# Kernel tuning notes

Hardware: AMD Instinct MI355X
Metric: run time of the kernel (lower is better)

## Reference

```python
import jax, jax.numpy as jnp
import numpy as np

B, C, H, W = 8, 96, 56, 56
N = H * W
K = 9
COUT = 2 * C  # 192


def setup_inputs() -> dict:
    key = jax.random.key(0)
    ks = jax.random.split(key, 12)
    s = 0.05
    inp = {
        "x": jax.random.normal(ks[0], (B, C, H, W), jnp.float32),
        "kmap_w": jax.random.normal(ks[1], (C, 500), jnp.float32) * s,
        "kmap_b": jnp.zeros((500,), jnp.float32),
        "kfc_w": jax.random.normal(ks[2], (500, 64), jnp.float32) * s,
        "kfc_b": jnp.zeros((64,), jnp.float32),
        "kmu_w": jax.random.normal(ks[3], (64, 32), jnp.float32) * s,
        "kmu_b": jnp.zeros((32,), jnp.float32),
        "kdec_w": jax.random.normal(ks[4], (32, K), jnp.float32) * s,
        "kdec_b": jnp.zeros((K,), jnp.float32),
        "ec1_w": jax.random.normal(ks[5], (2 * C, C), jnp.float32) * s,
        "ec1_b": jnp.zeros((C,), jnp.float32),
        "ec2_w": jax.random.normal(ks[6], (2 * C, C), jnp.float32) * s,
        "ec2_b": jnp.zeros((C,), jnp.float32),
        "fc_w": jax.random.normal(ks[7], (C, COUT), jnp.float32) * s,
        "fc_b": jnp.zeros((COUT,), jnp.float32),
        "io_w": jax.random.normal(ks[8], (C, COUT), jnp.float32) * s,
        "io_b": jnp.zeros((COUT,), jnp.float32),
        "up_w": jax.random.normal(ks[9], (2 * COUT, COUT), jnp.float32) * s,
        "up_b": jnp.zeros((COUT,), jnp.float32),
    }
    return inp


def reference(x, kmap_w, kmap_b, kfc_w, kfc_b, kmu_w, kmu_b, kdec_w, kdec_b,
              ec1_w, ec1_b, ec2_w, ec2_b, fc_w, fc_b, io_w, io_b, up_w, up_b):
    b, c, h, w = x.shape
    n = h * w
    xf = x.reshape(b, c, n).transpose(0, 2, 1)  # [B, N, C]

    # ---- dense kNN graph (dilation=1, deterministic) ----
    sq = jnp.sum(xf * xf, axis=-1)  # [B, N]
    dist = sq[:, :, None] - 2.0 * jnp.einsum('bnc,bmc->bnm', xf, xf) + sq[:, None, :]
    _, nn_idx = jax.lax.top_k(-dist, K)  # [B, N, K] local neighbor indices

    nodes = xf.reshape(b * n, c)  # flat node features

    # ---- VAE-like K predictor -> per-node kept-degree (non-differentiable) ----
    hK = nodes @ kmap_w + kmap_b
    hK = jax.nn.relu(hK @ kfc_w + kfc_b)
    mu = hK @ kmu_w + kmu_b
    logits = mu @ kdec_w + kdec_b  # [B*N, K]
    k_int = jnp.argmax(logits, axis=1)  # in [0, K-1]

    # edge mask: keep first k_int[i] of node i's K edges
    edge_mask = (jnp.arange(K)[None, :] < k_int[:, None]).reshape(-1)  # [B*N*K]
    emask = edge_mask.astype(nodes.dtype)[:, None]

    # flatten edges with per-batch node offsets (local -> global indices)
    offs = (jnp.arange(b) * n)[:, None, None]
    src = (nn_idx + offs).reshape(-1)              # x_j
    dst = jnp.repeat(jnp.arange(b * n), K)         # x_i (center)

    def edge_conv(feat, wgt, bias):
        xi = feat[dst]
        xj = feat[src]
        msg = jnp.concatenate([xi, xj - xi], axis=-1) @ wgt + bias
        msg = msg * emask  # pruned edges contribute 0 to 'add' aggregation
        return jax.ops.segment_sum(msg, dst, num_segments=b * n)

    h1 = jax.nn.relu(edge_conv(nodes, ec1_w, ec1_b))
    h2 = edge_conv(h1, ec2_w, ec2_b)
    agg = h2 @ fc_w + fc_b                 # EdgeAgg output [B*N, COUT]

    xio = nodes @ io_w + io_b              # inOutFC
    upd = jax.nn.relu(jnp.concatenate([xio, agg], axis=-1) @ up_w + up_b)

    out = upd.reshape(b, n, 2 * c).transpose(0, 2, 1).reshape(b, 2 * c, h, w)
    return out
```

## Files before the change

kernel.cpp:

```cpp
#include <hip/hip_runtime.h>

#define NODES 25088
#define NB 8
#define NPB 3136
#define C 96
#define KNN 9
#define COUT 192
#define MSPLIT 4
#define T12 12
#define NCAND (MSPLIT * T12)

typedef float f32x4 __attribute__((ext_vector_type(4)));
typedef float f32x16 __attribute__((ext_vector_type(16)));
typedef short s16x8 __attribute__((ext_vector_type(8)));

__device__ __forceinline__ unsigned short f2bf(float x) {
  unsigned u = __float_as_uint(x);
  return (unsigned short)((u + 0x7fffu + ((u >> 16) & 1u)) >> 16);
}
__device__ __forceinline__ float bf2f(unsigned short h) {
  return __uint_as_float(((unsigned)h) << 16);
}

__global__ __launch_bounds__(256) void txsq_kernel(
    const float* __restrict__ x, float* __restrict__ xf, float* __restrict__ sq,
    unsigned short* __restrict__ xh, unsigned short* __restrict__ xl) {
  __shared__ float t[96][33];
  int tid = threadIdx.x;
  int b = blockIdx.y;
  int n0 = blockIdx.x * 32;
  const float* xb = x + (size_t)b * C * NPB;
  int tn = tid & 31, tc = tid >> 5;
#pragma unroll
  for (int i = 0; i < 12; i++) {
    int c = tc + i * 8;
    t[c][tn] = xb[(size_t)c * NPB + n0 + tn];
  }
  __syncthreads();
#pragma unroll
  for (int k = 0; k < 3; k++) {
    int it = tid + k * 256;
    int nl = it / 24, c4 = it % 24;
    int node = b * NPB + n0 + nl;
    float4 v;
    v.x = t[4 * c4 + 0][nl];
    v.y = t[4 * c4 + 1][nl];
    v.z = t[4 * c4 + 2][nl];
    v.w = t[4 * c4 + 3][nl];
    ushort4 h, l;
    h.x = f2bf(v.x); l.x = f2bf(v.x - bf2f(h.x));
    h.y = f2bf(v.y); l.y = f2bf(v.y - bf2f(h.y));
    h.z = f2bf(v.z); l.z = f2bf(v.z - bf2f(h.z));
    h.w = f2bf(v.w); l.w = f2bf(v.w - bf2f(h.w));
    ((float4*)(xf + (size_t)node * C))[c4] = v;
    ((ushort4*)(xh + (size_t)node * C))[c4] = h;
    ((ushort4*)(xl + (size_t)node * C))[c4] = l;
  }
  if (tid < 32) {
    int node = b * NPB + n0 + tid;
    float s = 0.f;
#pragma unroll
    for (int i = 0; i < 24; i++) {
      float4 v;
      v.x = t[4 * i + 0][tid];
      v.y = t[4 * i + 1][tid];
      v.z = t[4 * i + 2][tid];
      v.w = t[4 * i + 3][tid];
      s += v.x * v.x + v.y * v.y + v.z * v.z + v.w * v.w;
    }
    sq[node] = s;
  }
}

__global__ void fold_all_kernel(
    const float* __restrict__ kmap_w, const float* __restrict__ kmap_b,
    const float* __restrict__ kfc_w, const float* __restrict__ kfc_b,
    const float* __restrict__ kmu_w, const float* __restrict__ kmu_b,
    const float* __restrict__ kdec_w, const float* __restrict__ kdec_b,
    const float* __restrict__ ec1_w, const float* __restrict__ ec2_w,
    const float* __restrict__ io_w, const float* __restrict__ io_b,
    const float* __restrict__ fc_w, const float* __restrict__ fc_b,
    const float* __restrict__ up_w, const float* __restrict__ up_b,
    float* __restrict__ WkP, float* __restrict__ bkP, float* __restrict__ WdP,
    float* __restrict__ bdP, float* __restrict__ bPf,
    unsigned short* __restrict__ B1h, unsigned short* __restrict__ B1l,
    unsigned short* __restrict__ B2h, unsigned short* __restrict__ B2l,
    unsigned short* __restrict__ BFh, unsigned short* __restrict__ BFl) {
  __shared__ float sh[4][64];
  int bid = blockIdx.x, tid = threadIdx.x;
  int tx = tid & 63, ty = tid >> 6;
  if (bid < 96) {
    int m = bid;
    float acc = 0.f;
    for (int k = ty; k < 500; k += 4) acc += kmap_w[m * 500 + k] * kfc_w[k * 64 + tx];
    sh[ty][tx] = acc;
    __syncthreads();
    if (ty == 0) WkP[m * 64 + tx] = sh[0][tx] + sh[1][tx] + sh[2][tx] + sh[3][tx];
  } else if (bid == 96) {
    float acc = 0.f;
    for (int k = ty; k < 500; k += 4) acc += kmap_b[k] * kfc_w[k * 64 + tx];
    sh[ty][tx] = acc;
    __syncthreads();
    if (ty == 0) bkP[tx] = sh[0][tx] + sh[1][tx] + sh[2][tx] + sh[3][tx] + kfc_b[tx];
  } else if (bid < 161) {
    int m = bid - 97;
    float acc = 0.f;
    if (tx < 9) {
      for (int k = ty; k < 32; k += 4) acc += kmu_w[m * 32 + k] * kdec_w[k * 9 + tx];
    }
    sh[ty][tx] = acc;
    __syncthreads();
    if (ty == 0 && tx < 9) WdP[m * 9 + tx] = sh[0][tx] + sh[1][tx] + sh[2][tx] + sh[3][tx];
  } else if (bid == 161) {
    float acc = 0.f;
    if (tx < 9) {
      for (int k = ty; k < 32; k += 4) acc += kmu_b[k] * kdec_w[k * 9 + tx];
    }
    sh[ty][tx] = acc;
    __syncthreads();
    if (ty == 0 && tx < 9) bdP[tx] = sh[0][tx] + sh[1][tx] + sh[2][tx] + sh[3][tx] + kdec_b[tx];
  } else if (bid < 234) {
    int t = (bid - 162) * 256 + tid;
    int n = t / 192, k = t % 192;
    float v = ec1_w[(size_t)k * 96 + n];
    if (k < 96) v -= ec1_w[(size_t)(k + 96) * 96 + n];
    unsigned short h = f2bf(v);
    B1h[t] = h;
    B1l[t] = f2bf(v - bf2f(h));
  } else if (bid < 306) {
    int t = (bid - 234) * 256 + tid;
    int n = t / 192, k = t % 192;
    float v = ec2_w[(size_t)k * 96 + n];
    if (k < 96) v -= ec2_w[(size_t)(k + 96) * 96 + n];
    unsigned short h = f2bf(v);
    B2h[t] = h;
    B2l[t] = f2bf(v - bf2f(h));
  } else if (bid < 594) {
    int r = bid - 306;
    int m = r / 3, n = (r % 3) * 64 + tx;
    float acc = 0.f;
    for (int k = ty; k < 192; k += 4) acc += io_w[m * 192 + k] * up_w[(size_t)k * 192 + n];
    sh[ty][tx] = acc;
    __syncthreads();
    if (ty == 0) {
      float v = sh[0][tx] + sh[1][tx] + sh[2][tx] + sh[3][tx];
      unsigned short h = f2bf(v);
      BFh[(size_t)n * 192 + m] = h;
      BFl[(size_t)n * 192 + m] = f2bf(v - bf2f(h));
    }
  } else if (bid < 882) {
    int r = bid - 594;
    int m = r / 3, n = (r % 3) * 64 + tx;
    float acc = 0.f;
    for (int k = ty; k < 192; k += 4)
      acc += fc_w[m * 192 + k] * up_w[(size_t)(192 + k) * 192 + n];
    sh[ty][tx] = acc;
    __syncthreads();
    if (ty == 0) {
      float v = sh[0][tx] + sh[1][tx] + sh[2][tx] + sh[3][tx];
      unsigned short h = f2bf(v);
      BFh[(size_t)n * 192 + 96 + m] = h;
      BFl[(size_t)n * 192 + 96 + m] = f2bf(v - bf2f(h));
    }
  } else {
    if (tid < 192) {
      float acc = up_b[tid];
      for (int k = 0; k < 192; k++) {
        acc += io_b[k] * up_w[k * 192 + tid];
        acc += fc_b[k] * up_w[(192 + k) * 192 + tid];
      }
      bPf[tid] = acc;
    }
  }
}

__global__ __launch_bounds__(256) void gemmhead_kernel(
    const float* __restrict__ A0, const float* __restrict__ B,
    const float* __restrict__ bias, const float* __restrict__ WdP,
    const float* __restrict__ bdP, int* __restrict__ kint,
    float* __restrict__ rs) {
  __shared__ float As[16][68];
  __shared__ float Bs[16][68];
  __shared__ float hs[64][68];
  __shared__ float wd[576];
  __shared__ float bd[9];
  int tid = threadIdx.x;
  int tx = tid & 15, ty = tid >> 4;
  int row0 = blockIdx.x * 64;
  for (int f = tid; f < 576; f += 256) wd[f] = WdP[f];
  if (tid < 9) bd[tid] = bdP[tid];
  float acc[4][4] = {};
  int ai = tid >> 2;
  int ak = (tid & 3) * 4;
  int bk = tid >> 4;
  int bj = (tid & 15) * 4;

  for (int k0 = 0; k0 < 96; k0 += 16) {
    {
      int r = row0 + ai;
      float4 v = *(const float4*)(A0 + (size_t)r * 96 + k0 + ak);
      As[ak + 0][ai] = v.x;
      As[ak + 1][ai] = v.y;
      As[ak + 2][ai] = v.z;
      As[ak + 3][ai] = v.w;
    }
    {
      int kg = k0 + bk;
      float4 v = *(const float4*)(B + (size_t)kg * 64 + bj);
      *(float4*)&Bs[bk][bj] = v;
    }
    __syncthreads();
#pragma unroll
    for (int kk = 0; kk < 16; kk++) {
      float4 av = *(const float4*)&As[kk][ty * 4];
      float4 bv = *(const float4*)&Bs[kk][tx * 4];
      acc[0][0] += av.x * bv.x; acc[0][1] += av.x * bv.y; acc[0][2] += av.x * bv.z; acc[0][3] += av.x * bv.w;
      acc[1][0] += av.y * bv.x; acc[1][1] += av.y * bv.y; acc[1][2] += av.y * bv.z; acc[1][3] += av.y * bv.w;
      acc[2][0] += av.z * bv.x; acc[2][1] += av.z * bv.y; acc[2][2] += av.z * bv.z; acc[2][3] += av.z * bv.w;
      acc[3][0] += av.w * bv.x; acc[3][1] += av.w * bv.y; acc[3][2] += av.w * bv.z; acc[3][3] += av.w * bv.w;
    }
    __syncthreads();
  }
#pragma unroll
  for (int ii = 0; ii < 4; ii++) {
#pragma unroll
    for (int jj = 0; jj < 4; jj++) {
      int j = tx * 4 + jj;
      hs[ty * 4 + ii][j] = fmaxf(acc[ii][jj] + bias[j], 0.f);
    }
  }
  __syncthreads();
  if (tid < 64) {
    int node = row0 + tid;
    const float4* hp = (const float4*)hs[tid];
    float4 h[16];
#pragma unroll
    for (int i = 0; i < 16; i++) h[i] = hp[i];
    float best = -3.4e38f;
    int bi = 0;
#pragma unroll
    for (int n = 0; n < 9; n++) {
      float a = bd[n];
#pragma unroll
      for (int k = 0; k < 16; k++) {
        float4 hv = h[k];
        a += hv.x * wd[(4 * k + 0) * 9 + n] + hv.y * wd[(4 * k + 1) * 9 + n] +
             hv.z * wd[(4 * k + 2) * 9 + n] + hv.w * wd[(4 * k + 3) * 9 + n];
      }
      if (a > best) { best = a; bi = n; }
    }
    kint[node] = bi;
    rs[node] = (float)bi;
  }
}

__device__ __forceinline__ void ce(float& a, float& b) {
  float lo = fminf(a, b);
  b = fmaxf(a, b);
  a = lo;
}

__device__ __forceinline__ void sort16(float* s) {
  ce(s[0], s[1]); ce(s[2], s[3]); ce(s[0], s[2]); ce(s[1], s[3]); ce(s[1], s[2]);
  ce(s[4], s[5]); ce(s[6], s[7]); ce(s[4], s[6]); ce(s[5], s[7]); ce(s[5], s[6]);
  ce(s[0], s[4]); ce(s[1], s[5]); ce(s[2], s[6]); ce(s[3], s[7]);
  ce(s[2], s[4]); ce(s[3], s[5]);
  ce(s[1], s[2]); ce(s[3], s[4]); ce(s[5], s[6]);
  ce(s[8], s[9]); ce(s[10], s[11]); ce(s[8], s[10]); ce(s[9], s[11]); ce(s[9], s[10]);
  ce(s[12], s[13]); ce(s[14], s[15]); ce(s[12], s[14]); ce(s[13], s[15]); ce(s[13], s[14]);
  ce(s[8], s[12]); ce(s[9], s[13]); ce(s[10], s[14]); ce(s[11], s[15]);
  ce(s[10], s[12]); ce(s[11], s[13]);
  ce(s[9], s[10]); ce(s[11], s[12]); ce(s[13], s[14]);
  ce(s[0], s[8]); ce(s[1], s[9]); ce(s[2], s[10]); ce(s[3], s[11]);
  ce(s[4], s[12]); ce(s[5], s[13]); ce(s[6], s[14]); ce(s[7], s[15]);
  ce(s[4], s[8]); ce(s[5], s[9]); ce(s[6], s[10]); ce(s[7], s[11]);
  ce(s[2], s[4]); ce(s[3], s[5]); ce(s[6], s[8]); ce(s[7], s[9]);
  ce(s[10], s[12]); ce(s[11], s[13]);
  ce(s[1], s[2]); ce(s[3], s[4]); ce(s[5], s[6]); ce(s[7], s[8]);
  ce(s[9], s[10]); ce(s[11], s[12]); ce(s[13], s[14]);
}

__device__ __forceinline__ void bmerge12(float* fd, const float* s) {
  float L[12];
#pragma unroll
  for (int i = 0; i < 12; i++) L[i] = fminf(fd[i], s[11 - i]);
  ce(L[0], L[8]); ce(L[1], L[9]); ce(L[2], L[10]); ce(L[3], L[11]);
  ce(L[4], L[8]); ce(L[5], L[9]); ce(L[6], L[10]); ce(L[7], L[11]);
  ce(L[0], L[2]); ce(L[1], L[3]); ce(L[4], L[6]); ce(L[5], L[7]);
  ce(L[8], L[10]); ce(L[9], L[11]);
  ce(L[0], L[1]); ce(L[2], L[3]); ce(L[4], L[5]); ce(L[6], L[7]);
  ce(L[8], L[9]); ce(L[10], L[11]);
#pragma unroll
  for (int i = 0; i < 12; i++) fd[i] = L[i];
}

__global__ __launch_bounds__(256) void knn_mfma_kernel(
    const unsigned short* __restrict__ xh, const unsigned short* __restrict__ xl,
    const float* __restrict__ sq, int* __restrict__ pk_i) {
  __shared__ __align__(16) float smem_f[6784];
  unsigned short* mhA = (unsigned short*)smem_f;
  unsigned short* mhB = (unsigned short*)(smem_f + 3328);
  float* sqsA = smem_f + 6656;
  float* sqsB = smem_f + 6720;
  int tid = threadIdx.x;
  int lane = tid & 63, wv = tid >> 6;
  int wm = wv >> 1, wq = wv & 1;
  int b = blockIdx.y, z = blockIdx.z;
  int q0 = blockIdx.x * 64;
  int bbase = b * NPB;
  int t0 = (z * 49) / MSPLIT, t1 = ((z + 1) * 49) / MSPLIT;

  int koff = (lane >> 5) * 8;
  int qrow = bbase + q0 + wq * 32 + (lane & 31);
  s16x8 bqh[6], bql[6];
  {
    const unsigned short* ph = xh + (size_t)qrow * 96 + koff;
    const unsigned short* pl = xl + (size_t)qrow * 96 + koff;
#pragma unroll
    for (int kc = 0; kc < 6; kc++) {
      bqh[kc] = *(const s16x8*)(ph + kc * 16);
      bql[kc] = *(const s16x8*)(pl + kc * 16);
    }
  }
  float sqr = sq[qrow];

  float fd[12];
#pragma unroll
  for (int k = 0; k < 12; k++) fd[k] = 3.4e38f;

  int srow = tid >> 1;
  int tloc = srow >> 6;
  int rrow = srow & 63;
  int sseg = (tid & 1) * 48;
  int soff = rrow * 104 + sseg;
  unsigned short* mhd = tloc ? mhB : mhA;

  s16x8 st[6];
  float stq = 0.f;
  {
    int tA = t0 + tloc;
    int ts = (tA < t1) ? tA : (t1 - 1);
    const unsigned short* gh = xh + (size_t)(bbase + ts * 64 + rrow) * 96 + sseg;
#pragma unroll
    for (int i = 0; i < 6; i++) st[i] = *(const s16x8*)(gh + i * 8);
    if (tid < 128) {
      int tq = t0 + (tid >> 6);
      int tqs = (tq < t1) ? tq : (t1 - 1);
      stq = sq[bbase + tqs * 64 + (tid & 63)];
    }
  }

  int sqbase = wm * 32 + 4 * (lane >> 5);
  int mrow = wm * 32 + (lane & 31);
  int np = (t1 - t0 + 1) >> 1;

  for (int p = 0; p < np; p++) {
    int ta = t0 + 2 * p, tb = ta + 1;
    __syncthreads();
#pragma unroll
    for (int i = 0; i < 6; i++) *(s16x8*)(mhd + soff + i * 8) = st[i];
    if (tid < 128) ((tid >> 6) ? sqsB : sqsA)[tid & 63] = stq;
    __syncthreads();

    {
      int tn = t0 + 2 * (p + 1) + tloc;
      int ts = (tn < t1) ? tn : (t1 - 1);
      const unsigned short* gh = xh + (size_t)(bbase + ts * 64 + rrow) * 96 + sseg;
#pragma unroll
      for (int i = 0; i < 6; i++) st[i] = *(const s16x8*)(gh + i * 8);
      if (tid < 128) {
        int tq = t0 + 2 * (p + 1) + (tid >> 6);
        int tqs = (tq < t1) ? tq : (t1 - 1);
        stq = sq[bbase + tqs * 64 + (tid & 63)];
      }
    }

    {
      f32x16 acc = (f32x16){0.f, 0.f, 0.f, 0.f, 0.f, 0.f, 0.f, 0.f,
                            0.f, 0.f, 0.f, 0.f, 0.f, 0.f, 0.f, 0.f};
#pragma unroll
      for (int kc = 0; kc < 6; kc++) {
        s16x8 amh = *(const s16x8*)(mhA + mrow * 104 + kc * 16 + koff);
        acc = __builtin_amdgcn_mfma_f32_32x32x16_bf16(amh, bqh[kc], acc, 0, 0, 0);
        acc = __builtin_amdgcn_mfma_f32_32x32x16_bf16(amh, bql[kc], acc, 0, 0, 0);
      }
      f32x4 sm0 = *(const f32x4*)(sqsA + sqbase);
      f32x4 sm1 = *(const f32x4*)(sqsA + sqbase + 8);
      f32x4 sm2 = *(const f32x4*)(sqsA + sqbase + 16);
      f32x4 sm3 = *(const f32x4*)(sqsA + sqbase + 24);
      int lbase = (ta - t0) * 64;
      float cs[16];
#pragma unroll
      for (int reg = 0; reg < 16; reg++) {
        int g = reg >> 2, e = reg & 3;
        float sqm = (g == 0) ? sm0[e] : (g == 1) ? sm1[e] : (g == 2) ? sm2[e] : sm3[e];
        int mloc = wm * 32 + e + 8 * g + 4 * (lane >> 5);
        float d = fmaf(-2.f, acc[reg], sqr + sqm);
        unsigned u = (__float_as_uint(d) & 0xFFFFFC00u) | (unsigned)(lbase + mloc);
        cs[reg] = __uint_as_float(u);
      }
      sort16(cs);
      bmerge12(fd, cs);
    }
    if (tb < t1) {
      f32x16 acc = (f32x16){0.f, 0.f, 0.f, 0.f, 0.f, 0.f, 0.f, 0.f,
                            0.f, 0.f, 0.f, 0.f, 0.f, 0.f, 0.f, 0.f};
#pragma unroll
      for (int kc = 0; kc < 6; kc++) {
        s16x8 amh = *(const s16x8*)(mhB + mrow * 104 + kc * 16 + koff);
        acc = __builtin_amdgcn_mfma_f32_32x32x16_bf16(amh, bqh[kc], acc, 0, 0, 0);
        acc = __builtin_amdgcn_mfma_f32_32x32x16_bf16(amh, bql[kc], acc, 0, 0, 0);
      }
      f32x4 sm0 = *(const f32x4*)(sqsB + sqbase);
      f32x4 sm1 = *(const f32x4*)(sqsB + sqbase + 8);
      f32x4 sm2 = *(const f32x4*)(sqsB + sqbase + 16);
      f32x4 sm3 = *(const f32x4*)(sqsB + sqbase + 24);
      int lbase = (tb - t0) * 64;
      float cs[16];
#pragma unroll
      for (int reg = 0; reg < 16; reg++) {
        int g = reg >> 2, e = reg & 3;
        float sqm = (g == 0) ? sm0[e] : (g == 1) ? sm1[e] : (g == 2) ? sm2[e] : sm3[e];
        int mloc = wm * 32 + e + 8 * g + 4 * (lane >> 5);
        float d = fmaf(-2.f, acc[reg], sqr + sqm);
        unsigned u = (__float_as_uint(d) & 0xFFFFFC00u) | (unsigned)(lbase + mloc);
        cs[reg] = __uint_as_float(u);
      }
      sort16(cs);
      bmerge12(fd, cs);
    }
  }

  __syncthreads();
  float* cd = smem_f;
#pragma unroll
  for (int k = 0; k < 12; k++) cd[(wv * 64 + lane) * 13 + k] = fd[k];
  __syncthreads();
  if (wv == 0) {
    int wva = lane >> 5, ql = lane & 31;
    int ra = wva * 64 + ql, rb = wva * 64 + ql + 32;
    int rc = (wva + 2) * 64 + ql, rd = (wva + 2) * 64 + ql + 32;
    float A[12], B[12];
#pragma unroll
    for (int k = 0; k < 12; k++) { A[k] = cd[ra * 13 + k]; B[k] = cd[rb * 13 + k]; }
    bmerge12(A, B);
    float Cc[12], Dd[12];
#pragma unroll
    for (int k = 0; k < 12; k++) { Cc[k] = cd[rc * 13 + k]; Dd[k] = cd[rd * 13 + k]; }
    bmerge12(Cc, Dd);
    bmerge12(A, Cc);
    size_t base = ((size_t)(bbase + q0 + lane) * MSPLIT + z) * T12;
#pragma unroll
    for (int k = 0; k < T12; k++) {
      int mloc = (int)(__float_as_uint(A[k]) & 0x3FFu) + t0 * 64;
      pk_i[base + k] = bbase + mloc;
    }
  }
}

__global__ __launch_bounds__(256) void rescore_kernel(
    const float* __restrict__ xf, const float* __restrict__ sq,
    const int* __restrict__ pk_i, int* __restrict__ nn) {
  __shared__ float qr[4][96];
  __shared__ float sqq[4];
  int tid = threadIdx.x;
  int qloc = tid >> 6, c = tid & 63;
  int qbase = blockIdx.x * 4;
  for (int f = tid; f < 4 * 96; f += 256)
    qr[f / 96][f % 96] = xf[(size_t)(qbase + f / 96) * 96 + f % 96];
  if (tid < 4) sqq[tid] = sq[qbase + tid];
  __syncthreads();

  int q = qbase + qloc;
  int jv = 0;
  if (c < NCAND) jv = pk_i[(size_t)q * NCAND + c];

  int grp = c >> 3;
  int chunk = c & 7;
  const float4* qp = (const float4*)qr[qloc];
  float4 qv0 = qp[chunk];
  float4 qv1 = qp[chunk + 8];
  float4 qv2 = qp[chunk + 16];

  float dots[6];
#pragma unroll
  for (int it = 0; it < 6; it++) {
    int j = __shfl(jv, it * 8 + grp, 64);
    const float4* mp = (const float4*)(xf + (size_t)j * 96);
    float4 m0 = mp[chunk];
    float4 m1 = mp[chunk + 8];
    float4 m2 = mp[chunk + 16];
    float p = qv0.x * m0.x + qv0.y * m0.y + qv0.z * m0.z + qv0.w * m0.w +
              qv1.x * m1.x + qv1.y * m1.y + qv1.z * m1.z + qv1.w * m1.w +
              qv2.x * m2.x + qv2.y * m2.y + qv2.z * m2.z + qv2.w * m2.w;
    p += __shfl_xor(p, 1, 64);
    p += __shfl_xor(p, 2, 64);
    p += __shfl_xor(p, 4, 64);
    dots[it] = p;
  }

  float g0 = __shfl(dots[0], (c & 7) * 8, 64);
  float g1 = __shfl(dots[1], (c & 7) * 8, 64);
  float g2 = __shfl(dots[2], (c & 7) * 8, 64);
  float g3 = __shfl(dots[3], (c & 7) * 8, 64);
  float g4 = __shfl(dots[4], (c & 7) * 8, 64);
  float g5 = __shfl(dots[5], (c & 7) * 8, 64);
  int itstar = c >> 3;
  float dot = g0;
  dot = (itstar == 1) ? g1 : dot;
  dot = (itstar == 2) ? g2 : dot;
  dot = (itstar == 3) ? g3 : dot;
  dot = (itstar == 4) ? g4 : dot;
  dot = (itstar == 5) ? g5 : dot;

  unsigned long long key = 0xFFFFFFFFFFFFFFFFull;
  if (c < NCAND) {
    float d = (sqq[qloc] - 2.0f * dot) + sq[jv];
    unsigned u = __float_as_uint(d);
    u ^= (u & 0x80000000u) ? 0xFFFFFFFFu : 0x80000000u;
    key = ((unsigned long long)u << 32) | (unsigned)jv;
  }

#pragma unroll
  for (int k = 2; k <= 64; k <<= 1) {
#pragma unroll
    for (int jm = k >> 1; jm >= 1; jm >>= 1) {
      unsigned long long other = __shfl_xor(key, jm, 64);
      bool takeMin = ((c & jm) == 0) == ((c & k) == 0);
      bool sw = (other < key) == takeMin;
      key = sw ? other : key;
    }
  }

  if (c < KNN) {
    nn[(size_t)q * KNN + c] = (int)(unsigned)(key & 0xFFFFFFFFull);
  }
}

__global__ __launch_bounds__(192) void mfma_ec_fused_kernel(
    const unsigned short* __restrict__ A0h, const unsigned short* __restrict__ A0l,
    const float* __restrict__ feat32, const unsigned short* __restrict__ gfh,
    const unsigned short* __restrict__ gfl, int mode,
    const int* __restrict__ nn, const int* __restrict__ kint,
    const unsigned short* __restrict__ Bth, const unsigned short* __restrict__ Btl,
    const float* __restrict__ rs, const float* __restrict__ bias, int relu,
    unsigned short* __restrict__ Oh, unsigned short* __restrict__ Ol) {
  __shared__ float rsL[32];
  __shared__ float bL[96];
  __shared__ __align__(16) unsigned short Sth[32][104];
  __shared__ __align__(16) unsigned short Stl[32][104];
  int tid = threadIdx.x, lane = tid & 63, wv = tid >> 6;
  int m0 = blockIdx.x * 32;
  if (tid < 32) rsL[tid] = rs[m0 + tid];
  if (tid < 96) bL[tid] = bias[tid];

  for (int it = tid; it < 768; it += 192) {
    int nl = it / 24, c4 = it % 24;
    int node = m0 + nl;
    int kc = kint[node];
    const int* nr = nn + (size_t)node * KNN;
    float4 acc = make_float4(0.f, 0.f, 0.f, 0.f);
    if (mode == 0) {
      for (int k = 0; k < kc; k++) {
        int j = nr[k];
        float4 v = ((const float4*)(feat32 + (size_t)j * C))[c4];
        acc.x += v.x; acc.y += v.y; acc.z += v.z; acc.w += v.w;
      }
    } else {
      for (int k = 0; k < kc; k++) {
        int j = nr[k];
        ushort4 h = ((const ushort4*)(gfh + (size_t)j * C))[c4];
        ushort4 l = ((const ushort4*)(gfl + (size_t)j * C))[c4];
        acc.x += bf2f(h.x) + bf2f(l.x);
        acc.y += bf2f(h.y) + bf2f(l.y);
        acc.z += bf2f(h.z) + bf2f(l.z);
        acc.w += bf2f(h.w) + bf2f(l.w);
      }
    }
    ushort4 h, l;
    h.x = f2bf(acc.x); l.x = f2bf(acc.x - bf2f(h.x));
    h.y = f2bf(acc.y); l.y = f2bf(acc.y - bf2f(h.y));
    h.z = f2bf(acc.z); l.z = f2bf(acc.z - bf2f(h.z));
    h.w = f2bf(acc.w); l.w = f2bf(acc.w - bf2f(h.w));
    *(ushort4*)&Sth[nl][c4 * 4] = h;
    *(ushort4*)&Stl[nl][c4 * 4] = l;
  }
  __syncthreads();

  int koff = (lane >> 5) * 8;
  int arow = m0 + (lane & 31);
  const unsigned short* a0h = A0h + (size_t)arow * 96 + koff;
  const unsigned short* a0l = A0l + (size_t)arow * 96 + koff;
  int rloc = lane & 31;
  int n = wv * 32 + (lane & 31);

  f32x16 acc1 = (f32x16){0.f, 0.f, 0.f, 0.f, 0.f, 0.f, 0.f, 0.f,
                         0.f, 0.f, 0.f, 0.f, 0.f, 0.f, 0.f, 0.f};
  f32x16 acc2 = acc1;

#pragma unroll
  for (int c = 0; c < 6; c++) {
    s16x8 ah = *(const s16x8*)(a0h + c * 16);
    s16x8 al = *(const s16x8*)(a0l + c * 16);
    size_t bo = (size_t)n * 192 + c * 16 + koff;
    s16x8 bh = *(const s16x8*)(Bth + bo);
    s16x8 bl = *(const s16x8*)(Btl + bo);
    acc1 = __builtin_amdgcn_mfma_f32_32x32x16_bf16(ah, bh, acc1, 0, 0, 0);
    acc1 = __builtin_amdgcn_mfma_f32_32x32x16_bf16(al, bh, acc1, 0, 0, 0);
    acc1 = __builtin_amdgcn_mfma_f32_32x32x16_bf16(ah, bl, acc1, 0, 0, 0);
  }
#pragma unroll
  for (int c = 6; c < 12; c++) {
    s16x8 ah = *(const s16x8*)(&Sth[rloc][(c - 6) * 16 + koff]);
    s16x8 al = *(const s16x8*)(&Stl[rloc][(c - 6) * 16 + koff]);
    size_t bo = (size_t)n * 192 + c * 16 + koff;
    s16x8 bh = *(const s16x8*)(Bth + bo);
    s16x8 bl = *(const s16x8*)(Btl + bo);
    acc2 = __builtin_amdgcn_mfma_f32_32x32x16_bf16(ah, bh, acc2, 0, 0, 0);
    acc2 = __builtin_amdgcn_mfma_f32_32x32x16_bf16(al, bh, acc2, 0, 0, 0);
    acc2 = __builtin_amdgcn_mfma_f32_32x32x16_bf16(ah, bl, acc2, 0, 0, 0);
  }

  float bn = bL[n];
#pragma unroll
  for (int reg = 0; reg < 16; reg++) {
    int rl = (reg & 3) + 8 * (reg >> 2) + 4 * (lane >> 5);
    int r = m0 + rl;
    float v = rsL[rl] * (acc1[reg] + bn) + acc2[reg];
    if (relu) v = fmaxf(v, 0.f);
    unsigned short h = f2bf(v);
    Oh[(size_t)r * 96 + n] = h;
    Ol[(size_t)r * 96 + n] = f2bf(v - bf2f(h));
  }
}

__global__ __launch_bounds__(192) void mfma_final_kernel(
    const unsigned short* __restrict__ A0h, const unsigned short* __restrict__ A0l,
    const unsigned short* __restrict__ A1h, const unsigned short* __restrict__ A1l,
    const unsigned short* __restrict__ Bth, const unsigned short* __restrict__ Btl,
    const float* __restrict__ bias, float* __restrict__ out) {
  __shared__ float bL[96];
  __shared__ float tt[3][32][33];
  int tid = threadIdx.x, lane = tid & 63, wv = tid >> 6;
  int m0 = blockIdx.x * 32;
  int n0 = blockIdx.y * 96;
  if (tid < 96) bL[tid] = bias[n0 + tid];
  __syncthreads();

  int koff = (lane >> 5) * 8;
  int arow = m0 + (lane & 31);
  const unsigned short* a0h = A0h + (size_t)arow * 96 + koff;
  const unsigned short* a0l = A0l + (size_t)arow * 96 + koff;
  const unsigned short* a1h = A1h + (size_t)arow * 96 + koff;
  const unsigned short* a1l = A1l + (size_t)arow * 96 + koff;
  int nloc = lane & 31;
  int n = n0 + wv * 32 + nloc;

  f32x16 acc = (f32x16){0.f, 0.f, 0.f, 0.f, 0.f, 0.f, 0.f, 0.f,
                        0.f, 0.f, 0.f, 0.f, 0.f, 0.f, 0.f, 0.f};
#pragma unroll
  for (int c = 0; c < 12; c++) {
    s16x8 ah, al;
    if (c < 6) {
      ah = *(const s16x8*)(a0h + c * 16);
      al = *(const s16x8*)(a0l + c * 16);
    } else {
      ah = *(const s16x8*)(a1h + (c - 6) * 16);
      al = *(const s16x8*)(a1l + (c - 6) * 16);
    }
    size_t bo = (size_t)n * 192 + c * 16 + koff;
    s16x8 bh = *(const s16x8*)(Bth + bo);
    s16x8 bl = *(const s16x8*)(Btl + bo);
    acc = __builtin_amdgcn_mfma_f32_32x32x16_bf16(ah, bh, acc, 0, 0, 0);
    acc = __builtin_amdgcn_mfma_f32_32x32x16_bf16(al, bh, acc, 0, 0, 0);
    acc = __builtin_amdgcn_mfma_f32_32x32x16_bf16(ah, bl, acc, 0, 0, 0);
  }

  float bn = bL[wv * 32 + nloc];
#pragma unroll
  for (int reg = 0; reg < 16; reg++) {
    int rl = (reg & 3) + 8 * (reg >> 2) + 4 * (lane >> 5);
    tt[wv][nloc][rl] = fmaxf(acc[reg] + bn, 0.f);
  }
  __builtin_amdgcn_s_waitcnt(0);
  int gbase = m0 + nloc;
  int bb = gbase / NPB, nidx = gbase % NPB;
#pragma unroll
  for (int i = 0; i < 16; i++) {
    int nl = 2 * i + (lane >> 5);
    float v = tt[wv][nl][nloc];
    int ng = n0 + wv * 32 + nl;
    out[(size_t)bb * COUT * NPB + (size_t)ng * NPB + nidx] = v;
  }
}

extern "C" void kernel_launch(void* const* d_in, const int* in_sizes, int n_in,
                              void* d_out, int out_size, void* d_ws, size_t ws_size,
                              hipStream_t stream) {
  const float* x      = (const float*)d_in[0];
  const float* kmap_w = (const float*)d_in[1];
  const float* kmap_b = (const float*)d_in[2];
  const float* kfc_w  = (const float*)d_in[3];
  const float* kfc_b  = (const float*)d_in[4];
  const float* kmu_w  = (const float*)d_in[5];
  const float* kmu_b  = (const float*)d_in[6];
  const float* kdec_w = (const float*)d_in[7];
  const float* kdec_b = (const float*)d_in[8];
  const float* ec1_w  = (const float*)d_in[9];
  const float* ec1_b  = (const float*)d_in[10];
  const float* ec2_w  = (const float*)d_in[11];
  const float* ec2_b  = (const float*)d_in[12];
  const float* fc_w   = (const float*)d_in[13];
  const float* fc_b   = (const float*)d_in[14];
  const float* io_w   = (const float*)d_in[15];
  const float* io_b   = (const float*)d_in[16];
  const float* up_w   = (const float*)d_in[17];
  const float* up_b   = (const float*)d_in[18];

  char* ws = (char*)d_ws;
  size_t off = 0;
  auto alloc = [&](size_t bytes) -> void* {
    void* p = ws + off;
    off += (bytes + 255) & ~(size_t)255;
    return p;
  };
  const size_t HBF = (size_t)NODES * C * 2;
  float* xf   = (float*)alloc((size_t)NODES * C * 4);
  float* sqb  = (float*)alloc((size_t)NODES * 4);
  float* rs   = (float*)alloc((size_t)NODES * 4);
  int*   kint = (int*)alloc((size_t)NODES * 4);
  int*   nn   = (int*)alloc((size_t)NODES * KNN * 4);
  unsigned short* xh = (unsigned short*)alloc(HBF);
  unsigned short* xl = (unsigned short*)alloc(HBF);
  char* region = (char*)alloc((size_t)NODES * COUT * 4);
  int*   pk_i   = (int*)region;
  unsigned short* h1h = (unsigned short*)region;
  unsigned short* h1l = (unsigned short*)(region + HBF);
  unsigned short* h2h = (unsigned short*)(region + 2 * HBF);
  unsigned short* h2l = (unsigned short*)(region + 3 * HBF);
  float* WkP = (float*)alloc(96 * 64 * 4);
  float* bkP = (float*)alloc(64 * 4);
  float* WdP = (float*)alloc(64 * 9 * 4);
  float* bdP = (float*)alloc(16 * 4);
  float* bPf = (float*)alloc(192 * 4);
  unsigned short* B1h = (unsigned short*)alloc(96 * 192 * 2);
  unsigned short* B1l = (unsigned short*)alloc(96 * 192 * 2);
  unsigned short* B2h = (unsigned short*)alloc(96 * 192 * 2);
  unsigned short* B2l = (unsigned short*)alloc(96 * 192 * 2);
  unsigned short* BFh = (unsigned short*)alloc(192 * 192 * 2);
  unsigned short* BFl = (unsigned short*)alloc(192 * 192 * 2);

  txsq_kernel<<<dim3(98, 8), 256, 0, stream>>>(x, xf, sqb, xh, xl);

  fold_all_kernel<<<883, 256, 0, stream>>>(
      kmap_w, kmap_b, kfc_w, kfc_b, kmu_w, kmu_b, kdec_w, kdec_b, ec1_w, ec2_w,
      io_w, io_b, fc_w, fc_b, up_w, up_b,
      WkP, bkP, WdP, bdP, bPf, B1h, B1l, B2h, B2l, BFh, BFl);

  gemmhead_kernel<<<392, 256, 0, stream>>>(xf, WkP, bkP, WdP, bdP, kint, rs);

  knn_mfma_kernel<<<dim3(49, 8, MSPLIT), 256, 0, stream>>>(xh, xl, sqb, pk_i);
  rescore_kernel<<<6272, 256, 0, stream>>>(xf, sqb, pk_i, nn);

  mfma_ec_fused_kernel<<<784, 192, 0, stream>>>(
      xh, xl, xf, (const unsigned short*)nullptr, (const unsigned short*)nullptr,
      0, nn, kint, B1h, B1l, rs, ec1_b, 1, h1h, h1l);
  mfma_ec_fused_kernel<<<784, 192, 0, stream>>>(
      h1h, h1l, (const float*)nullptr, h1h, h1l,
      1, nn, kint, B2h, B2l, rs, ec2_b, 0, h2h, h2l);
  mfma_final_kernel<<<dim3(784, 2), 192, 0, stream>>>(xh, xl, h2h, h2l, BFh, BFl,
                                                      bPf, (float*)d_out);
}
```

Measured before the change: 329.2 us.

## Read kNN candidate tiles straight from global memory instead of LDS staging

The kNN MFMA kernel no longer stages candidate tiles and squared norms in double-buffered shared memory behind __syncthreads. Each wave now loads the A fragments and norms directly from global (L2-cached) memory and walks alternating tiles by parity, covering both 32-row halves itself. This removes the per-tile barriers and LDS store/load traffic, so waves run independently. The cost is more global/L2 load traffic, since each candidate tile is now read by two waves, and load latency is no longer hidden by a software prefetch.

Measured after the change: 339.5 us. +3.1%, slower.

```diff
diff --git a/kernel.cpp b/kernel.cpp
--- a/kernel.cpp
+++ b/kernel.cpp
@@ -297,21 +297,17 @@
 __global__ __launch_bounds__(256) void knn_mfma_kernel(
     const unsigned short* __restrict__ xh, const unsigned short* __restrict__ xl,
     const float* __restrict__ sq, int* __restrict__ pk_i) {
-  __shared__ __align__(16) float smem_f[6784];
-  unsigned short* mhA = (unsigned short*)smem_f;
-  unsigned short* mhB = (unsigned short*)(smem_f + 3328);
-  float* sqsA = smem_f + 6656;
-  float* sqsB = smem_f + 6720;
+  __shared__ __align__(16) float cd[256 * 13];
   int tid = threadIdx.x;
   int lane = tid & 63, wv = tid >> 6;
-  int wm = wv >> 1, wq = wv & 1;
+  int qh = wv & 1, par = wv >> 1;
   int b = blockIdx.y, z = blockIdx.z;
   int q0 = blockIdx.x * 64;
   int bbase = b * NPB;
   int t0 = (z * 49) / MSPLIT, t1 = ((z + 1) * 49) / MSPLIT;
 
   int koff = (lane >> 5) * 8;
-  int qrow = bbase + q0 + wq * 32 + (lane & 31);
+  int qrow = bbase + q0 + qh * 32 + (lane & 31);
   s16x8 bqh[6], bql[6];
   {
     const unsigned short* ph = xh + (size_t)qrow * 96 + koff;
@@ -328,73 +324,35 @@
 #pragma unroll
   for (int k = 0; k < 12; k++) fd[k] = 3.4e38f;
 
-  int srow = tid >> 1;
-  int tloc = srow >> 6;
-  int rrow = srow & 63;
-  int sseg = (tid & 1) * 48;
-  int soff = rrow * 104 + sseg;
-  unsigned short* mhd = tloc ? mhB : mhA;
-
-  s16x8 st[6];
-  float stq = 0.f;
-  {
-    int tA = t0 + tloc;
-    int ts = (tA < t1) ? tA : (t1 - 1);
-    const unsigned short* gh = xh + (size_t)(bbase + ts * 64 + rrow) * 96 + sseg;
-#pragma unroll
-    for (int i = 0; i < 6; i++) st[i] = *(const s16x8*)(gh + i * 8);
-    if (tid < 128) {
-      int tq = t0 + (tid >> 6);
-      int tqs = (tq < t1) ? tq : (t1 - 1);
-      stq = sq[bbase + tqs * 64 + (tid & 63)];
-    }
-  }
-
-  int sqbase = wm * 32 + 4 * (lane >> 5);
-  int mrow = wm * 32 + (lane & 31);
-  int np = (t1 - t0 + 1) >> 1;
-
-  for (int p = 0; p < np; p++) {
-    int ta = t0 + 2 * p, tb = ta + 1;
-    __syncthreads();
-#pragma unroll
-    for (int i = 0; i < 6; i++) *(s16x8*)(mhd + soff + i * 8) = st[i];
-    if (tid < 128) ((tid >> 6) ? sqsB : sqsA)[tid & 63] = stq;
-    __syncthreads();
-
-    {
-      int tn = t0 + 2 * (p + 1) + tloc;
-      int ts = (tn < t1) ? tn : (t1 - 1);
-      const unsigned short* gh = xh + (size_t)(bbase + ts * 64 + rrow) * 96 + sseg;
-#pragma unroll
-      for (int i = 0; i < 6; i++) st[i] = *(const s16x8*)(gh + i * 8);
-      if (tid < 128) {
-        int tq = t0 + 2 * (p + 1) + (tid >> 6);
-        int tqs = (tq < t1) ? tq : (t1 - 1);
-        stq = sq[bbase + tqs * 64 + (tid & 63)];
-      }
-    }
-
-    {
+  int lgrp = 4 * (lane >> 5);
+  int arow_lane = lane & 31;
+
+  for (int t = t0 + par; t < t1; t += 2) {
+    int m0 = bbase + t * 64;
+    int lbase = (t - t0) * 64;
+#pragma unroll
+    for (int mh = 0; mh < 2; mh++) {
+      const unsigned short* ah =
+          xh + (size_t)(m0 + mh * 32 + arow_lane) * 96 + koff;
       f32x16 acc = (f32x16){0.f, 0.f, 0.f, 0.f, 0.f, 0.f, 0.f, 0.f,
                             0.f, 0.f, 0.f, 0.f, 0.f, 0.f, 0.f, 0.f};
 #pragma unroll
       for (int kc = 0; kc < 6; kc++) {
-        s16x8 amh = *(const s16x8*)(mhA + mrow * 104 + kc * 16 + koff);
+        s16x8 amh = *(const s16x8*)(ah + kc * 16);
         acc = __builtin_amdgcn_mfma_f32_32x32x16_bf16(amh, bqh[kc], acc, 0, 0, 0);
         acc = __builtin_amdgcn_mfma_f32_32x32x16_bf16(amh, bql[kc], acc, 0, 0, 0);
       }
-      f32x4 sm0 = *(const f32x4*)(sqsA + sqbase);
-      f32x4 sm1 = *(const f32x4*)(sqsA + sqbase + 8);
-      f32x4 sm2 = *(const f32x4*)(sqsA + sqbase + 16);
-      f32x4 sm3 = *(const f32x4*)(sqsA + sqbase + 24);
-      int lbase = (ta - t0) * 64;
+      const float* sqp = sq + m0 + mh * 32 + lgrp;
+      f32x4 sm0 = *(const f32x4*)(sqp);
+      f32x4 sm1 = *(const f32x4*)(sqp + 8);
+      f32x4 sm2 = *(const f32x4*)(sqp + 16);
+      f32x4 sm3 = *(const f32x4*)(sqp + 24);
       float cs[16];
 #pragma unroll
       for (int reg = 0; reg < 16; reg++) {
         int g = reg >> 2, e = reg & 3;
         float sqm = (g == 0) ? sm0[e] : (g == 1) ? sm1[e] : (g == 2) ? sm2[e] : sm3[e];
-        int mloc = wm * 32 + e + 8 * g + 4 * (lane >> 5);
+        int mloc = mh * 32 + e + 8 * g + lgrp;
         float d = fmaf(-2.f, acc[reg], sqr + sqm);
         unsigned u = (__float_as_uint(d) & 0xFFFFFC00u) | (unsigned)(lbase + mloc);
         cs[reg] = __uint_as_float(u);
@@ -402,37 +360,8 @@
       sort16(cs);
       bmerge12(fd, cs);
     }
-    if (tb < t1) {
-      f32x16 acc = (f32x16){0.f, 0.f, 0.f, 0.f, 0.f, 0.f, 0.f, 0.f,
-                            0.f, 0.f, 0.f, 0.f, 0.f, 0.f, 0.f, 0.f};
-#pragma unroll
-      for (int kc = 0; kc < 6; kc++) {
-        s16x8 amh = *(const s16x8*)(mhB + mrow * 104 + kc * 16 + koff);
-        acc = __builtin_amdgcn_mfma_f32_32x32x16_bf16(amh, bqh[kc], acc, 0, 0, 0);
-        acc = __builtin_amdgcn_mfma_f32_32x32x16_bf16(amh, bql[kc], acc, 0, 0, 0);
-      }
-      f32x4 sm0 = *(const f32x4*)(sqsB + sqbase);
-      f32x4 sm1 = *(const f32x4*)(sqsB + sqbase + 8);
-      f32x4 sm2 = *(const f32x4*)(sqsB + sqbase + 16);
-      f32x4 sm3 = *(const f32x4*)(sqsB + sqbase + 24);
-      int lbase = (tb - t0) * 64;
-      float cs[16];
-#pragma unroll
-      for (int reg = 0; reg < 16; reg++) {
-        int g = reg >> 2, e = reg & 3;
-        float sqm = (g == 0) ? sm0[e] : (g == 1) ? sm1[e] : (g == 2) ? sm2[e] : sm3[e];
-        int mloc = wm * 32 + e + 8 * g + 4 * (lane >> 5);
-        float d = fmaf(-2.f, acc[reg], sqr + sqm);
-        unsigned u = (__float_as_uint(d) & 0xFFFFFC00u) | (unsigned)(lbase + mloc);
-        cs[reg] = __uint_as_float(u);
-      }
-      sort16(cs);
-      bmerge12(fd, cs);
-    }
-  }
-
-  __syncthreads();
-  float* cd = smem_f;
+  }
+
 #pragma unroll
   for (int k = 0; k < 12; k++) cd[(wv * 64 + lane) * 13 + k] = fd[k];
   __syncthreads();
```
